# Kernel tuning notes

Hardware: AMD Instinct MI355X
Metric: run time of the kernel (lower is better)

## Reference

```python
import jax, jax.numpy as jnp
import numpy as np

B, T, I, H, O = 64, 2048, 256, 256, 128

def _rnn_scan(xp, W_hh):
    # xp: [T, B, H] = precomputed W_ih @ x + b_ih + b_hh per timestep
    h0 = jnp.zeros((xp.shape[1], W_hh.shape[0]), xp.dtype)
    def step(h, xt):
        h_new = jnp.tanh(xt + h @ W_hh.T)
        return h_new, h_new
    _, hs = jax.lax.scan(step, h0, xp)
    return hs  # [T, B, H]

def setup_inputs() -> dict:
    key = jax.random.key(0)
    ks = jax.random.split(key, 9)
    s1 = 1.0 / np.sqrt(H)
    s2 = 1.0 / np.sqrt(O)
    return {
        "x": jax.random.normal(ks[0], (B, T, I), dtype=jnp.float32),
        "W_ih1": jax.random.normal(ks[1], (H, I), dtype=jnp.float32) * s1,
        "W_hh1": jax.random.normal(ks[2], (H, H), dtype=jnp.float32) * s1,
        "b_ih1": jax.random.normal(ks[3], (H,), dtype=jnp.float32) * s1,
        "b_hh1": jax.random.normal(ks[4], (H,), dtype=jnp.float32) * s1,
        "W_ih2": jax.random.normal(ks[5], (O, H), dtype=jnp.float32) * s2,
        "W_hh2": jax.random.normal(ks[6], (O, O), dtype=jnp.float32) * s2,
        "b_ih2": jax.random.normal(ks[7], (O,), dtype=jnp.float32) * s2,
        "b_hh2": jax.random.normal(ks[8], (O,), dtype=jnp.float32) * s2,
    }

def reference(x, W_ih1, W_hh1, b_ih1, b_hh1, W_ih2, W_hh2, b_ih2, b_hh2):
    # Layer 1: h_t = tanh(W_ih1 x_t + b_ih1 + W_hh1 h_{t-1} + b_hh1)
    xp1 = jnp.einsum('bti,hi->tbh', x, W_ih1) + (b_ih1 + b_hh1)
    h1 = _rnn_scan(xp1, W_hh1)                      # [T, B, H]
    # Layer 2: o_t = tanh(W_ih2 h_t + b_ih2 + W_hh2 o_{t-1} + b_hh2)
    xp2 = jnp.einsum('tbh,oh->tbo', h1, W_ih2) + (b_ih2 + b_hh2)
    h2 = _rnn_scan(xp2, W_hh2)                      # [T, B, O]
    out = jnp.transpose(h2, (1, 0, 2)).reshape(-1, O)  # [B*T, num_classes]
    return out
```

## Files before the change

kernel.cpp:

```cpp
#include <hip/hip_runtime.h>
#include <math.h>

#define BB 64
#define TT 2048
#define II 256
#define HH 256
#define OO 128

typedef __attribute__((ext_vector_type(4))) float f32x4;

template<int N>
__global__ __launch_bounds__(256)
void gemm_bias(const float* __restrict__ A, const float* __restrict__ W,
               const float* __restrict__ b1, const float* __restrict__ b2,
               float* __restrict__ C)
{
    constexpr int K = 256;
    __shared__ float sA[16][132];
    __shared__ float sB[16][132];
    const int tid  = threadIdx.x;
    const long row0 = (long)blockIdx.x * 128;
    const int  col0 = blockIdx.y * 128;

    const int tm = tid & 15;
    const int tn = tid >> 4;

    float acc[8][8];
#pragma unroll
    for (int i = 0; i < 8; ++i)
#pragma unroll
        for (int j = 0; j < 8; ++j) acc[i][j] = 0.f;

    const int f0  = tid;
    const int f1  = tid + 256;
    const int am0 = f0 >> 2, ak0 = (f0 & 3) * 4;
    const int am1 = f1 >> 2, ak1 = (f1 & 3) * 4;

    for (int kt = 0; kt < K; kt += 16) {
        float4 a0 = *(const float4*)&A[(row0 + am0) * K + kt + ak0];
        float4 a1 = *(const float4*)&A[(row0 + am1) * K + kt + ak1];
        float4 w0 = *(const float4*)&W[(long)(col0 + am0) * K + kt + ak0];
        float4 w1 = *(const float4*)&W[(long)(col0 + am1) * K + kt + ak1];
        __syncthreads();
        sA[ak0+0][am0] = a0.x; sA[ak0+1][am0] = a0.y; sA[ak0+2][am0] = a0.z; sA[ak0+3][am0] = a0.w;
        sA[ak1+0][am1] = a1.x; sA[ak1+1][am1] = a1.y; sA[ak1+2][am1] = a1.z; sA[ak1+3][am1] = a1.w;
        sB[ak0+0][am0] = w0.x; sB[ak0+1][am0] = w0.y; sB[ak0+2][am0] = w0.z; sB[ak0+3][am0] = w0.w;
        sB[ak1+0][am1] = w1.x; sB[ak1+1][am1] = w1.y; sB[ak1+2][am1] = w1.z; sB[ak1+3][am1] = w1.w;
        __syncthreads();
#pragma unroll
        for (int k = 0; k < 16; ++k) {
            float4 av0 = *(const float4*)&sA[k][tm * 8];
            float4 av1 = *(const float4*)&sA[k][tm * 8 + 4];
            float4 bv0 = *(const float4*)&sB[k][tn * 8];
            float4 bv1 = *(const float4*)&sB[k][tn * 8 + 4];
            float am[8] = {av0.x, av0.y, av0.z, av0.w, av1.x, av1.y, av1.z, av1.w};
            float bn[8] = {bv0.x, bv0.y, bv0.z, bv0.w, bv1.x, bv1.y, bv1.z, bv1.w};
#pragma unroll
            for (int i = 0; i < 8; ++i)
#pragma unroll
                for (int j = 0; j < 8; ++j)
                    acc[i][j] += am[i] * bn[j];
        }
    }

    float bias[8];
#pragma unroll
    for (int j = 0; j < 8; ++j) {
        int col = col0 + tn * 8 + j;
        bias[j] = b1[col] + b2[col];
    }
#pragma unroll
    for (int i = 0; i < 8; ++i) {
        long row = row0 + tm * 8 + i;
        float4 v0, v1;
        v0.x = acc[i][0] + bias[0]; v0.y = acc[i][1] + bias[1];
        v0.z = acc[i][2] + bias[2]; v0.w = acc[i][3] + bias[3];
        v1.x = acc[i][4] + bias[4]; v1.y = acc[i][5] + bias[5];
        v1.z = acc[i][6] + bias[6]; v1.w = acc[i][7] + bias[7];
        *(float4*)&C[row * N + col0 + tn * 8]     = v0;
        *(float4*)&C[row * N + col0 + tn * 8 + 4] = v1;
    }
}

__device__ __forceinline__ float fast_tanh(float x) {
    float e = __expf(2.f * x);
    return 1.f - 2.f / (e + 1.f);
}

#define LIGHT_BARRIER() do {                                       \
    asm volatile("s_waitcnt lgkmcnt(0)" ::: "memory");             \
    __builtin_amdgcn_s_barrier();                                  \
} while (0)

#define PIN4(v) asm volatile("" : "+v"((v).x), "+v"((v).y), "+v"((v).z), "+v"((v).w))

#define PAIRSUM(dst_, x_) do {                                         \
    float _t = (x_), _u = (x_);                                        \
    asm("v_permlane32_swap_b32 %0, %1" : "+v"(_t), "+v"(_u));          \
    (dst_) = _t + _u;                                                  \
} while (0)

__global__ __launch_bounds__(512, 2)
void rnn_pipe(const float* __restrict__ W_hh1,
              const float* __restrict__ W_ih2,
              const float* __restrict__ W_hh2,
              const float* __restrict__ b_ih2,
              const float* __restrict__ b_hh2,
              float* __restrict__ XH,
              float* __restrict__ out,
              int* __restrict__ flags)
{
    const int tid = threadIdx.x;
    const int g   = tid & 31;
    const int ks  = tid >> 5;
    const int kp  = ks >> 1;

    if (blockIdx.x < BB) {
        __shared__ float h_lds[256];
        __shared__ float part[8 * 256];
        const int b = blockIdx.x;

        float4 w[8][4];
#pragma unroll
        for (int r = 0; r < 8; ++r)
#pragma unroll
            for (int c = 0; c < 4; ++c)
                w[r][c] = *(const float4*)&W_hh1[(g * 8 + r) * 256 + ks * 16 + c * 4];
#pragma unroll
        for (int r = 0; r < 8; ++r)
#pragma unroll
            for (int c = 0; c < 4; ++c)
                PIN4(w[r][c]);

        float* rowp = XH + (long)b * TT * HH;
        float xpb[8];
#pragma unroll
        for (int j = 0; j < 8; ++j) xpb[j] = 0.f;
        if (tid < 256) {
            h_lds[tid] = 0.f;
#pragma unroll
            for (int j = 0; j < 8; ++j)
                xpb[j] = __builtin_nontemporal_load(&rowp[(long)j * HH + tid]);
        }
        const int ro = ((tid & 7) >> 2) * 128 + ((tid >> 3) << 2) + (tid & 3);
        LIGHT_BARRIER();

        for (int t0 = 0; t0 < TT; t0 += 8) {
#pragma unroll
            for (int j = 0; j < 8; ++j) {
                const int t = t0 + j;

                float a[8];
#pragma unroll
                for (int r = 0; r < 8; ++r) a[r] = 0.f;
#pragma unroll
                for (int c = 0; c < 4; ++c) {
                    float4 h4c = *(const float4*)&h_lds[ks * 16 + c * 4];
#pragma unroll
                    for (int r = 0; r < 8; ++r)
                        a[r] += w[r][c].x * h4c.x + w[r][c].y * h4c.y
                              + w[r][c].z * h4c.z + w[r][c].w * h4c.w;
                }

                float s[8];
#pragma unroll
                for (int r = 0; r < 8; ++r) PAIRSUM(s[r], a[r]);

                if (!(ks & 1))
                    *(float4*)&part[kp * 256 + g * 4] =
                        make_float4(s[0], s[1], s[2], s[3]);
                else
                    *(float4*)&part[kp * 256 + 128 + g * 4] =
                        make_float4(s[4], s[5], s[6], s[7]);
                LIGHT_BARRIER();

                if (tid < 256) {
                    float r0 = part[0 * 256 + ro] + part[1 * 256 + ro]
                             + part[2 * 256 + ro] + part[3 * 256 + ro];
                    float r1 = part[4 * 256 + ro] + part[5 * 256 + ro]
                             + part[6 * 256 + ro] + part[7 * 256 + ro];
                    float v = fast_tanh((r0 + r1) + xpb[j]);
                    h_lds[tid] = v;
                    __builtin_nontemporal_store(v, &rowp[(long)t * HH + tid]);
                }
                if (j < 7) LIGHT_BARRIER();
            }

            asm volatile("s_waitcnt vmcnt(0) lgkmcnt(0)" ::: "memory");
            __builtin_amdgcn_s_barrier();
            if (tid == 0)
                __hip_atomic_store(&flags[b], t0 + 8, __ATOMIC_RELEASE,
                                   __HIP_MEMORY_SCOPE_AGENT);

            if (tid < 256 && t0 + 8 < TT) {
#pragma unroll
                for (int j = 0; j < 8; ++j)
                    xpb[j] = __builtin_nontemporal_load(
                        &rowp[(long)(t0 + 8 + j) * HH + tid]);
            }
        }
    } else {
        __shared__ float h1_lds[256];
        __shared__ float o_lds[128];
        __shared__ float part2[8 * 132];
        __shared__ int   seen_sh;
        const int b = blockIdx.x - BB;

        float4 wi[4][4];
        float4 wh[4][2];
#pragma unroll
        for (int r = 0; r < 4; ++r) {
#pragma unroll
            for (int c = 0; c < 4; ++c)
                wi[r][c] = *(const float4*)&W_ih2[(g * 4 + r) * 256 + ks * 16 + c * 4];
#pragma unroll
            for (int c = 0; c < 2; ++c)
                wh[r][c] = *(const float4*)&W_hh2[(g * 4 + r) * 128 + ks * 8 + c * 4];
        }
#pragma unroll
        for (int r = 0; r < 4; ++r) {
#pragma unroll
            for (int c = 0; c < 4; ++c) PIN4(wi[r][c]);
#pragma unroll
            for (int c = 0; c < 2; ++c) PIN4(wh[r][c]);
        }

        float bias = 0.f;
        if (tid < 128) {
            bias = b_ih2[tid] + b_hh2[tid];
            o_lds[tid] = 0.f;
        }
        const float* h1p = XH + (long)b * TT * HH;
        float* outp      = out + (long)b * TT * OO;
        LIGHT_BARRIER();

        int seen = 0;
        f32x4 pf = {0.f, 0.f, 0.f, 0.f};
        for (int t0 = 0; t0 < TT; t0 += 8) {
            if (seen < t0 + 8) {
                if (tid == 0) {
                    int s;
                    do {
                        s = __hip_atomic_load(&flags[b], __ATOMIC_RELAXED,
                                              __HIP_MEMORY_SCOPE_AGENT);
                    } while (s < t0 + 8);
                    s = __hip_atomic_load(&flags[b], __ATOMIC_ACQUIRE,
                                          __HIP_MEMORY_SCOPE_AGENT);
                    seen_sh = s;
                }
                LIGHT_BARRIER();
                seen = seen_sh;
            }
            if (tid < 64)
                pf = __builtin_nontemporal_load(
                    (const f32x4*)&h1p[(long)t0 * HH + tid * 4]);

            for (int j = 0; j < 8; ++j) {
                const int t = t0 + j;
                if (tid < 64) {
                    *(f32x4*)&h1_lds[tid * 4] = pf;
                    if (j < 7)
                        pf = __builtin_nontemporal_load(
                            (const f32x4*)&h1p[(long)(t + 1) * HH + tid * 4]);
                }
                LIGHT_BARRIER();

                float a2[4];
#pragma unroll
                for (int r = 0; r < 4; ++r) a2[r] = 0.f;
#pragma unroll
                for (int c = 0; c < 4; ++c) {
                    float4 h4c = *(const float4*)&h1_lds[ks * 16 + c * 4];
#pragma unroll
                    for (int r = 0; r < 4; ++r)
                        a2[r] += wi[r][c].x * h4c.x + wi[r][c].y * h4c.y
                               + wi[r][c].z * h4c.z + wi[r][c].w * h4c.w;
                }
#pragma unroll
                for (int c = 0; c < 2; ++c) {
                    float4 o4c = *(const float4*)&o_lds[ks * 8 + c * 4];
#pragma unroll
                    for (int r = 0; r < 4; ++r)
                        a2[r] += wh[r][c].x * o4c.x + wh[r][c].y * o4c.y
                               + wh[r][c].z * o4c.z + wh[r][c].w * o4c.w;
                }

                float s2[4];
#pragma unroll
                for (int r = 0; r < 4; ++r) PAIRSUM(s2[r], a2[r]);

                if (!(ks & 1))
                    *(float4*)&part2[kp * 132 + g * 4] =
                        make_float4(s2[0], s2[1], s2[2], s2[3]);
                LIGHT_BARRIER();

                if (tid < 128) {
                    float s = bias;
#pragma unroll
                    for (int st = 0; st < 8; ++st)
                        s += part2[st * 132 + tid];
                    float v = fast_tanh(s);
                    o_lds[tid] = v;
                    __builtin_nontemporal_store(v, &outp[(long)t * OO + tid]);
                }
            }
        }
    }
}

extern "C" void kernel_launch(void* const* d_in, const int* in_sizes, int n_in,
                              void* d_out, int out_size, void* d_ws, size_t ws_size,
                              hipStream_t stream)
{
    const float* x     = (const float*)d_in[0];
    const float* W_ih1 = (const float*)d_in[1];
    const float* W_hh1 = (const float*)d_in[2];
    const float* b_ih1 = (const float*)d_in[3];
    const float* b_hh1 = (const float*)d_in[4];
    const float* W_ih2 = (const float*)d_in[5];
    const float* W_hh2 = (const float*)d_in[6];
    const float* b_ih2 = (const float*)d_in[7];
    const float* b_hh2 = (const float*)d_in[8];
    float* out = (float*)d_out;

    float* xp1 = (float*)d_ws;
    const size_t FLAG_OFF = (size_t)BB * TT * HH * sizeof(float);
    int* flags = (int*)((char*)d_ws + FLAG_OFF);

    const int M = BB * TT;

    (void)hipMemsetAsync(flags, 0, BB * sizeof(int), stream);

    dim3 gA(M / 128, HH / 128);
    gemm_bias<HH><<<gA, 256, 0, stream>>>(x, W_ih1, b_ih1, b_hh1, xp1);

    rnn_pipe<<<2 * BB, 512, 0, stream>>>(W_hh1, W_ih2, W_hh2, b_ih2, b_hh2,
                                         xp1, out, flags);
}
```

Baseline: 2.043 ms.

## Interleave two batch rows per block to overlap matvec and reduction phases

```diff
diff --git a/kernel.cpp b/kernel.cpp
--- a/kernel.cpp
+++ b/kernel.cpp
@@ -115,10 +115,11 @@
     const int ks  = tid >> 5;
     const int kp  = ks >> 1;
 
-    if (blockIdx.x < BB) {
-        __shared__ float h_lds[256];
-        __shared__ float part[8 * 256];
-        const int b = blockIdx.x;
+    if (blockIdx.x < BB / 2) {
+        __shared__ float hA[256], hB[256];
+        __shared__ float partA[8 * 256], partB[8 * 256];
+        const int pb = blockIdx.x;
+        const int bA = 2 * pb, bB = 2 * pb + 1;
 
         float4 w[8][4];
 #pragma unroll
@@ -132,79 +133,98 @@
             for (int c = 0; c < 4; ++c)
                 PIN4(w[r][c]);
 
-        float* rowp = XH + (long)b * TT * HH;
-        float xpb[8];
-#pragma unroll
-        for (int j = 0; j < 8; ++j) xpb[j] = 0.f;
+        float* rowpA = XH + (long)bA * TT * HH;
+        float* rowpB = XH + (long)bB * TT * HH;
+
+        float xpbA[8], xpbB[8];
+#pragma unroll
+        for (int j = 0; j < 8; ++j) { xpbA[j] = 0.f; xpbB[j] = 0.f; }
         if (tid < 256) {
-            h_lds[tid] = 0.f;
-#pragma unroll
-            for (int j = 0; j < 8; ++j)
-                xpb[j] = __builtin_nontemporal_load(&rowp[(long)j * HH + tid]);
-        }
+            hA[tid] = 0.f; hB[tid] = 0.f;
+#pragma unroll
+            for (int j = 0; j < 8; ++j) {
+                xpbA[j] = rowpA[(long)j * HH + tid];
+                xpbB[j] = rowpB[(long)j * HH + tid];
+            }
+        }
+        *(float4*)&partA[tid * 4] = make_float4(0.f, 0.f, 0.f, 0.f);
+
         const int ro = ((tid & 7) >> 2) * 128 + ((tid >> 3) << 2) + (tid & 3);
+
+        auto prod_partials = [&](const float* hbuf, float* pbuf) {
+            float a[8];
+#pragma unroll
+            for (int r = 0; r < 8; ++r) a[r] = 0.f;
+#pragma unroll
+            for (int c = 0; c < 4; ++c) {
+                float4 h4c = *(const float4*)&hbuf[ks * 16 + c * 4];
+#pragma unroll
+                for (int r = 0; r < 8; ++r)
+                    a[r] += w[r][c].x * h4c.x + w[r][c].y * h4c.y
+                          + w[r][c].z * h4c.z + w[r][c].w * h4c.w;
+            }
+            float s[8];
+#pragma unroll
+            for (int r = 0; r < 8; ++r) PAIRSUM(s[r], a[r]);
+            if (!(ks & 1))
+                *(float4*)&pbuf[kp * 256 + g * 4] =
+                    make_float4(s[0], s[1], s[2], s[3]);
+            else
+                *(float4*)&pbuf[kp * 256 + 128 + g * 4] =
+                    make_float4(s[4], s[5], s[6], s[7]);
+        };
+
         LIGHT_BARRIER();
 
         for (int t0 = 0; t0 < TT; t0 += 8) {
 #pragma unroll
             for (int j = 0; j < 8; ++j) {
                 const int t = t0 + j;
-
-                float a[8];
-#pragma unroll
-                for (int r = 0; r < 8; ++r) a[r] = 0.f;
-#pragma unroll
-                for (int c = 0; c < 4; ++c) {
-                    float4 h4c = *(const float4*)&h_lds[ks * 16 + c * 4];
-#pragma unroll
-                    for (int r = 0; r < 8; ++r)
-                        a[r] += w[r][c].x * h4c.x + w[r][c].y * h4c.y
-                              + w[r][c].z * h4c.z + w[r][c].w * h4c.w;
-                }
-
-                float s[8];
-#pragma unroll
-                for (int r = 0; r < 8; ++r) PAIRSUM(s[r], a[r]);
-
-                if (!(ks & 1))
-                    *(float4*)&part[kp * 256 + g * 4] =
-                        make_float4(s[0], s[1], s[2], s[3]);
-                else
-                    *(float4*)&part[kp * 256 + 128 + g * 4] =
-                        make_float4(s[4], s[5], s[6], s[7]);
+                prod_partials(hB, partB);
+                if (tid < 256) {
+                    float r0 = partA[0 * 256 + ro] + partA[1 * 256 + ro]
+                             + partA[2 * 256 + ro] + partA[3 * 256 + ro];
+                    float r1 = partA[4 * 256 + ro] + partA[5 * 256 + ro]
+                             + partA[6 * 256 + ro] + partA[7 * 256 + ro];
+                    float v = fast_tanh((r0 + r1) + xpbA[j]);
+                    hA[tid] = v;
+                    rowpA[(long)t * HH + tid] = v;
+                }
                 LIGHT_BARRIER();
-
+                if (t + 1 < TT) prod_partials(hA, partA);
                 if (tid < 256) {
-                    float r0 = part[0 * 256 + ro] + part[1 * 256 + ro]
-                             + part[2 * 256 + ro] + part[3 * 256 + ro];
-                    float r1 = part[4 * 256 + ro] + part[5 * 256 + ro]
-                             + part[6 * 256 + ro] + part[7 * 256 + ro];
-                    float v = fast_tanh((r0 + r1) + xpb[j]);
-                    h_lds[tid] = v;
-                    __builtin_nontemporal_store(v, &rowp[(long)t * HH + tid]);
-                }
-                if (j < 7) LIGHT_BARRIER();
+                    float r0 = partB[0 * 256 + ro] + partB[1 * 256 + ro]
+                             + partB[2 * 256 + ro] + partB[3 * 256 + ro];
+                    float r1 = partB[4 * 256 + ro] + partB[5 * 256 + ro]
+                             + partB[6 * 256 + ro] + partB[7 * 256 + ro];
+                    float v = fast_tanh((r0 + r1) + xpbB[j]);
+                    hB[tid] = v;
+                    rowpB[(long)t * HH + tid] = v;
+                }
+                LIGHT_BARRIER();
             }
 
             asm volatile("s_waitcnt vmcnt(0) lgkmcnt(0)" ::: "memory");
             __builtin_amdgcn_s_barrier();
             if (tid == 0)
-                __hip_atomic_store(&flags[b], t0 + 8, __ATOMIC_RELEASE,
+                __hip_atomic_store(&flags[pb], t0 + 8, __ATOMIC_RELEASE,
                                    __HIP_MEMORY_SCOPE_AGENT);
 
             if (tid < 256 && t0 + 8 < TT) {
 #pragma unroll
-                for (int j = 0; j < 8; ++j)
-                    xpb[j] = __builtin_nontemporal_load(
-                        &rowp[(long)(t0 + 8 + j) * HH + tid]);
+                for (int j = 0; j < 8; ++j) {
+                    xpbA[j] = rowpA[(long)(t0 + 8 + j) * HH + tid];
+                    xpbB[j] = rowpB[(long)(t0 + 8 + j) * HH + tid];
+                }
             }
         }
     } else {
-        __shared__ float h1_lds[256];
-        __shared__ float o_lds[128];
-        __shared__ float part2[8 * 132];
+        __shared__ float h1A[256], h1B[256];
+        __shared__ float oA[128], oB[128];
+        __shared__ float p2A[8 * 132], p2B[8 * 132];
         __shared__ int   seen_sh;
-        const int b = blockIdx.x - BB;
+        const int cb = blockIdx.x - BB / 2;
+        const int bA = 2 * cb, bB = 2 * cb + 1;
 
         float4 wi[4][4];
         float4 wh[4][2];
@@ -228,82 +248,109 @@
         float bias = 0.f;
         if (tid < 128) {
             bias = b_ih2[tid] + b_hh2[tid];
-            o_lds[tid] = 0.f;
-        }
-        const float* h1p = XH + (long)b * TT * HH;
-        float* outp      = out + (long)b * TT * OO;
+            oA[tid] = 0.f; oB[tid] = 0.f;
+        }
+        const float* h1pA = XH + (long)bA * TT * HH;
+        const float* h1pB = XH + (long)bB * TT * HH;
+        float* outpA = out + (long)bA * TT * OO;
+        float* outpB = out + (long)bB * TT * OO;
+
+        auto cons_partials = [&](const float* h1buf, const float* obuf,
+                                 float* pbuf) {
+            float a2[4];
+#pragma unroll
+            for (int r = 0; r < 4; ++r) a2[r] = 0.f;
+#pragma unroll
+            for (int c = 0; c < 4; ++c) {
+                float4 h4c = *(const float4*)&h1buf[ks * 16 + c * 4];
+#pragma unroll
+                for (int r = 0; r < 4; ++r)
+                    a2[r] += wi[r][c].x * h4c.x + wi[r][c].y * h4c.y
+                           + wi[r][c].z * h4c.z + wi[r][c].w * h4c.w;
+            }
+#pragma unroll
+            for (int c = 0; c < 2; ++c) {
+                float4 o4c = *(const float4*)&obuf[ks * 8 + c * 4];
+#pragma unroll
+                for (int r = 0; r < 4; ++r)
+                    a2[r] += wh[r][c].x * o4c.x + wh[r][c].y * o4c.y
+                           + wh[r][c].z * o4c.z + wh[r][c].w * o4c.w;
+            }
+            float s2[4];
+#pragma unroll
+            for (int r = 0; r < 4; ++r) PAIRSUM(s2[r], a2[r]);
+            if (!(ks & 1))
+                *(float4*)&pbuf[kp * 132 + g * 4] =
+                    make_float4(s2[0], s2[1], s2[2], s2[3]);
+        };
+
+        f32x4 pfA = {0.f, 0.f, 0.f, 0.f};
+        f32x4 pfB = {0.f, 0.f, 0.f, 0.f};
         LIGHT_BARRIER();
 
-        int seen = 0;
-        f32x4 pf = {0.f, 0.f, 0.f, 0.f};
         for (int t0 = 0; t0 < TT; t0 += 8) {
-            if (seen < t0 + 8) {
-                if (tid == 0) {
-                    int s;
-                    do {
-                        s = __hip_atomic_load(&flags[b], __ATOMIC_RELAXED,
-                                              __HIP_MEMORY_SCOPE_AGENT);
-                    } while (s < t0 + 8);
-                    s = __hip_atomic_load(&flags[b], __ATOMIC_ACQUIRE,
+            if (tid == 0) {
+                int s;
+                do {
+                    s = __hip_atomic_load(&flags[cb], __ATOMIC_RELAXED,
                                           __HIP_MEMORY_SCOPE_AGENT);
-                    seen_sh = s;
-                }
-                LIGHT_BARRIER();
-                seen = seen_sh;
-            }
-            if (tid < 64)
-                pf = __builtin_nontemporal_load(
-                    (const f32x4*)&h1p[(long)t0 * HH + tid * 4]);
-
+                } while (s < t0 + 8);
+                s = __hip_atomic_load(&flags[cb], __ATOMIC_ACQUIRE,
+                                      __HIP_MEMORY_SCOPE_AGENT);
+                seen_sh = s;
+            }
+            LIGHT_BARRIER();
+            (void)seen_sh;
+
+            if (tid < 64) {
+                f32x4 a0 = *(const f32x4*)&h1pA[(long)t0 * HH + tid * 4];
+                pfB = *(const f32x4*)&h1pB[(long)t0 * HH + tid * 4];
+                *(f32x4*)&h1A[tid * 4] = a0;
+                pfA = *(const f32x4*)&h1pA[(long)(t0 + 1) * HH + tid * 4];
+            }
+            LIGHT_BARRIER();
+
+#pragma unroll
             for (int j = 0; j < 8; ++j) {
                 const int t = t0 + j;
                 if (tid < 64) {
-                    *(f32x4*)&h1_lds[tid * 4] = pf;
+                    *(f32x4*)&h1B[tid * 4] = pfB;
                     if (j < 7)
-                        pf = __builtin_nontemporal_load(
-                            (const f32x4*)&h1p[(long)(t + 1) * HH + tid * 4]);
+                        pfB = *(const f32x4*)&h1pB[(long)(t + 1) * HH + tid * 4];
+                }
+                cons_partials(h1A, oA, p2A);
+                if (t > 0 && tid < 128) {
+                    float s = bias;
+#pragma unroll
+                    for (int st = 0; st < 8; ++st) s += p2B[st * 132 + tid];
+                    float v = fast_tanh(s);
+                    oB[tid] = v;
+                    __builtin_nontemporal_store(v, &outpB[(long)(t - 1) * OO + tid]);
                 }
                 LIGHT_BARRIER();
-
-                float a2[4];
-#pragma unroll
-                for (int r = 0; r < 4; ++r) a2[r] = 0.f;
-#pragma unroll
-                for (int c = 0; c < 4; ++c) {
-                    float4 h4c = *(const float4*)&h1_lds[ks * 16 + c * 4];
-#pragma unroll
-                    for (int r = 0; r < 4; ++r)
-                        a2[r] += wi[r][c].x * h4c.x + wi[r][c].y * h4c.y
-                               + wi[r][c].z * h4c.z + wi[r][c].w * h4c.w;
-                }
-#pragma unroll
-                for (int c = 0; c < 2; ++c) {
-                    float4 o4c = *(const float4*)&o_lds[ks * 8 + c * 4];
-#pragma unroll
-                    for (int r = 0; r < 4; ++r)
-                        a2[r] += wh[r][c].x * o4c.x + wh[r][c].y * o4c.y
-                               + wh[r][c].z * o4c.z + wh[r][c].w * o4c.w;
-                }
-
-                float s2[4];
-#pragma unroll
-                for (int r = 0; r < 4; ++r) PAIRSUM(s2[r], a2[r]);
-
-                if (!(ks & 1))
-                    *(float4*)&part2[kp * 132 + g * 4] =
-                        make_float4(s2[0], s2[1], s2[2], s2[3]);
-                LIGHT_BARRIER();
-
+                if (tid < 64 && j < 7) {
+                    *(f32x4*)&h1A[tid * 4] = pfA;
+                    if (j < 6)
+                        pfA = *(const f32x4*)&h1pA[(long)(t + 2) * HH + tid * 4];
+                }
+                cons_partials(h1B, oB, p2B);
                 if (tid < 128) {
                     float s = bias;
 #pragma unroll
-                    for (int st = 0; st < 8; ++st)
-                        s += part2[st * 132 + tid];
+                    for (int st = 0; st < 8; ++st) s += p2A[st * 132 + tid];
                     float v = fast_tanh(s);
-                    o_lds[tid] = v;
-                    __builtin_nontemporal_store(v, &outp[(long)t * OO + tid]);
-                }
-            }
+                    oA[tid] = v;
+                    __builtin_nontemporal_store(v, &outpA[(long)t * OO + tid]);
+                }
+                LIGHT_BARRIER();
+            }
+        }
+        if (tid < 128) {
+            float s = bias;
+#pragma unroll
+            for (int st = 0; st < 8; ++st) s += p2B[st * 132 + tid];
+            __builtin_nontemporal_store(fast_tanh(s),
+                                        &outpB[(long)(TT - 1) * OO + tid]);
         }
     }
 }
@@ -329,11 +376,11 @@
 
     const int M = BB * TT;
 
-    (void)hipMemsetAsync(flags, 0, BB * sizeof(int), stream);
+    (void)hipMemsetAsync(flags, 0, (BB / 2) * sizeof(int), stream);
 
     dim3 gA(M / 128, HH / 128);
     gemm_bias<HH><<<gA, 256, 0, stream>>>(x, W_ih1, b_ih1, b_hh1, xp1);
 
-    rnn_pipe<<<2 * BB, 512, 0, stream>>>(W_hh1, W_ih2, W_hh2, b_ih2, b_hh2,
-                                         xp1, out, flags);
+    rnn_pipe<<<BB, 512, 0, stream>>>(W_hh1, W_ih2, W_hh2, b_ih2, b_hh2,
+                                     xp1, out, flags);
 }
```

Result: slower. 3.096 ms (+51.5%).
